# Kernel tuning notes

Measured on AMD Instinct MI355X. Metric: run time of the kernel, lower is better.

Reference implementation:

```python
import jax, jax.numpy as jnp
import numpy as np


def setup_inputs() -> dict:
    key = jax.random.key(0)
    ks = jax.random.split(key, 7)
    C = 256
    Cqk = C // 8  # 32
    B, D, H, W = 4, 16, 16, 16
    s_in = 1.0 / np.sqrt(C)  # conv1x1 fan_in = C
    return {
        "x": jax.random.normal(ks[0], (B, C, D, H, W), dtype=jnp.float32),
        "Wq": jax.random.uniform(ks[1], (Cqk, C), jnp.float32, -s_in, s_in),
        "bq": jax.random.uniform(ks[2], (Cqk,), jnp.float32, -s_in, s_in),
        "Wk": jax.random.uniform(ks[3], (Cqk, C), jnp.float32, -s_in, s_in),
        "bk": jax.random.uniform(ks[4], (Cqk,), jnp.float32, -s_in, s_in),
        "Wv": jax.random.uniform(ks[5], (C, C), jnp.float32, -s_in, s_in),
        "bv": jax.random.uniform(ks[6], (C,), jnp.float32, -s_in, s_in),
    }


def reference(x, Wq, bq, Wk, bk, Wv, bv):
    B, C, D, H, W = x.shape
    N = D * H * W
    xf = x.reshape(B, C, N)  # [B, C, N]
    # 1x1x1 convs == per-voxel GEMMs over the channel dim
    q = jnp.einsum('oc,bcn->bon', Wq, xf) + bq[None, :, None]  # [B, Cqk, N]
    k = jnp.einsum('oc,bcn->bon', Wk, xf) + bk[None, :, None]  # [B, Cqk, N]
    v = jnp.einsum('oc,bcn->bon', Wv, xf) + bv[None, :, None]  # [B, C, N]
    # attention[b, n, m] = softmax_m( q[:, n] . k[:, m] )
    scores = jnp.einsum('bcn,bcm->bnm', q, k)  # [B, N, N]
    attn = jax.nn.softmax(scores, axis=-1)
    # out = value @ attention^T  -> out[b, c, n] = sum_m v[b,c,m] * attn[b,n,m]
    out = jnp.einsum('bcm,bnm->bcn', v, attn)
    return x + out.reshape(B, C, D, H, W)
```

## Files before the change

kernel.cpp:

```cpp
#include <hip/hip_runtime.h>
#include <math.h>

#define B_   4
#define C_   256
#define CQK  32
#define N_   4096
#define TQ   64
#define TM   64
#define HITERS ((N_ / 2) / TM)
#define PSS  72
#define VSH  (C_ * TM)
#define XT2  264
#define VOS  40

typedef __attribute__((ext_vector_type(8))) short short8;
typedef __attribute__((ext_vector_type(4))) short short4v;
typedef __attribute__((ext_vector_type(4))) float f32x4;
typedef __attribute__((ext_vector_type(2))) unsigned int uint2v;

#if __has_builtin(__builtin_amdgcn_exp2f)
#define EXP2F(x) __builtin_amdgcn_exp2f(x)
#else
#define EXP2F(x) exp2f(x)
#endif

typedef const __attribute__((address_space(1))) unsigned int* gas1_t;
typedef __attribute__((address_space(3))) unsigned int* las3_t;
__device__ __forceinline__ void gload_lds16(const unsigned short* g, unsigned short* l) {
    __builtin_amdgcn_global_load_lds((gas1_t)g, (las3_t)l, 16, 0, 0);
}

__device__ __forceinline__ unsigned short f2bf(float f) {
    unsigned u = __builtin_bit_cast(unsigned, f);
    u += 0x7fffu + ((u >> 16) & 1u);
    return (unsigned short)(u >> 16);
}
__device__ __forceinline__ float bf2f(unsigned short s) {
    return __builtin_bit_cast(float, (unsigned)s << 16);
}
__device__ __forceinline__ unsigned pack2bf(float a, float b) {
    unsigned ua = __builtin_bit_cast(unsigned, a) + 0x8000u;
    unsigned ub = __builtin_bit_cast(unsigned, b) + 0x8000u;
#if __has_builtin(__builtin_amdgcn_perm)
    return __builtin_amdgcn_perm(ub, ua, 0x07060302u);
#else
    return (ua >> 16) | (ub & 0xffff0000u);
#endif
}

__global__ __launch_bounds__(256) void cvt_w(
    const float* __restrict__ Wq, const float* __restrict__ bq,
    const float* __restrict__ Wk, const float* __restrict__ bk,
    const float* __restrict__ Wv, const float* __restrict__ bv,
    unsigned short* __restrict__ wbf, float* __restrict__ biasf)
{
    const float LOG2E = 1.4426950408889634f;
    const int r = blockIdx.x;
    const int t = threadIdx.x;
    const float* src = (r < 32) ? (Wq + r * C_)
                     : (r < 64) ? (Wk + (r - 32) * C_)
                                : (Wv + (r - 64) * C_);
    const float scale = (r < 32) ? LOG2E : 1.0f;
    wbf[r * C_ + t] = f2bf(src[t] * scale);
    if (t == 0)
        biasf[r] = (r < 32) ? bq[r] * LOG2E : (r < 64) ? bk[r - 32] : bv[r - 64];
}

__global__ __launch_bounds__(256, 2) void proj_qkv(
    const float* __restrict__ x, const unsigned short* __restrict__ wbf,
    const float* __restrict__ biasf,
    unsigned short* __restrict__ qb, unsigned short* __restrict__ kb,
    unsigned short* __restrict__ vb)
{
    __shared__ __align__(16) unsigned short xT[32 * XT2];
    __shared__ __align__(16) unsigned short vout[256 * VOS];
    __shared__ __align__(16) unsigned short qks[32 * 72];

    const int t    = threadIdx.x;
    const int w    = t >> 6;
    const int lane = t & 63;
    const int quad = lane >> 4;
    const int c16  = lane & 15;
    const int n0   = blockIdx.x * 32;
    const int b    = blockIdx.y;

    {
        const int c0 = (t >> 3) * 8;
        const int nq = t & 7;
        f32x4 xv[8];
#pragma unroll
        for (int i = 0; i < 8; ++i)
            xv[i] = *(const f32x4*)&x[((size_t)(b * C_) + c0 + i) * N_ + n0 + 4 * nq];
#pragma unroll
        for (int j = 0; j < 4; ++j) {
            short8 pk;
#pragma unroll
            for (int i = 0; i < 8; ++i) pk[i] = (short)f2bf(xv[i][j]);
            *(short8*)&xT[(4 * nq + j) * XT2 + c0] = pk;
        }
    }
    __syncthreads();

    f32x4 acc[5][2];
#pragma unroll
    for (int i = 0; i < 5; ++i)
#pragma unroll
        for (int nt = 0; nt < 2; ++nt) acc[i][nt] = (f32x4){0.f, 0.f, 0.f, 0.f};

    const unsigned short* wr = wbf + (size_t)(80 * w + c16) * C_ + quad * 8;

#pragma unroll
    for (int ks = 0; ks < 8; ++ks) {
        short8 af[5], bf[2];
#pragma unroll
        for (int i = 0; i < 5; ++i)
            af[i] = *(const short8*)(wr + (size_t)(16 * i) * C_ + 32 * ks);
#pragma unroll
        for (int nt = 0; nt < 2; ++nt)
            bf[nt] = *(const short8*)&xT[(16 * nt + c16) * XT2 + ks * 32 + quad * 8];
#pragma unroll
        for (int i = 0; i < 5; ++i)
#pragma unroll
            for (int nt = 0; nt < 2; ++nt)
                acc[i][nt] = __builtin_amdgcn_mfma_f32_16x16x32_bf16(af[i], bf[nt], acc[i][nt], 0, 0, 0);
    }

#pragma unroll
    for (int i = 0; i < 5; ++i) {
        const int OT = 5 * w + i;
        const int obase = OT * 16 + 4 * quad;
        const f32x4 bv4 = *(const f32x4*)&biasf[obase];
#pragma unroll
        for (int nt = 0; nt < 2; ++nt) {
            const int n = 16 * nt + c16;
            float vals[4];
#pragma unroll
            for (int r = 0; r < 4; ++r) vals[r] = acc[i][nt][r] + bv4[r];
            if (OT >= 4) {
#pragma unroll
                for (int r = 0; r < 4; ++r)
                    vout[(obase + r - 64) * VOS + n] = f2bf(vals[r]);
            } else {
                const int col = (OT < 2 ? 0 : 32) + (OT & 1) * 16 + 4 * quad;
                short4v pk;
#pragma unroll
                for (int r = 0; r < 4; ++r) pk[r] = (short)f2bf(vals[r]);
                *(short4v*)&qks[n * 72 + col] = pk;
            }
        }
    }
    __syncthreads();

#pragma unroll
    for (int p = 0; p < 4; ++p) {
        const int c   = 64 * p + (t >> 2);
        const int seg = t & 3;
        const short8 vv = *(const short8*)&vout[c * VOS + seg * 8];
        *(short8*)(vb + ((size_t)(b * C_) + c) * N_ + n0 + seg * 8) = vv;
    }
    if (w < 2) {
        unsigned short* dst = w ? kb : qb;
        const int coff = w ? 32 : 0;
#pragma unroll
        for (int h = 0; h < 2; ++h) {
            const int n = 16 * h + (lane >> 2);
            const int c = (lane & 3) * 8;
            const short8 v = *(const short8*)&qks[n * 72 + coff + c];
            *(short8*)(dst + ((size_t)(b * N_) + n0 + n) * 32 + c) = v;
        }
    }
}

__global__ __launch_bounds__(512, 4) void attn_kernel(
    const unsigned short* __restrict__ qg,
    const unsigned short* __restrict__ kg,
    const unsigned short* __restrict__ vg,
    float* __restrict__ outp,
    unsigned short* __restrict__ Op1,
    float* __restrict__ lp)
{
    __shared__ __align__(16) unsigned short vs[2 * VSH];
    __shared__ __align__(16) unsigned short ps[TQ * PSS];
    __shared__ float ls[4 * TQ];

    const int t    = threadIdx.x;
    const int w    = t >> 6;
    const int lane = t & 63;
    const int quad = lane >> 4;
    const int c16  = lane & 15;
    const int flat = blockIdx.x;
    const int half = flat & 1;
    const int b    = (flat >> 1) & 3;
    const int q0   = (flat >> 3) * TQ;
    const int kvb0 = half * (N_ / 2);
    const int f   = w & 3;
    const int qg_ = w >> 2;
    const int cs = w & 3;
    const int pg = w >> 2;

    const unsigned short* kbase = kg + (size_t)(b * N_) * 32;
    const unsigned short* vbase = vg + (size_t)(b * C_) * N_;

    short8 bq[2];
#pragma unroll
    for (int g = 0; g < 2; ++g)
        bq[g] = *(const short8*)(qg + ((size_t)(b * N_) + q0 + 16 * (2 * qg_ + g) + c16) * 32 + quad * 8);

    const int vrow  = lane >> 3;
    const int vslot = lane & 7;

    const size_t koff = (size_t)(16 * f + c16) * 32 + quad * 8;

#pragma unroll
    for (int p = 0; p < 4; ++p) {
        const int c = 32 * w + 8 * p + vrow;
        gload_lds16(vbase + (size_t)c * N_ + kvb0 + 8 * (vslot ^ (c & 7)),
                    &vs[(32 * w + 8 * p) * TM]);
    }
    short8 akpre = *(const short8*)(kbase + (size_t)kvb0 * 32 + koff);
    __syncthreads();

    f32x4 O[4][2];
#pragma unroll
    for (int ct = 0; ct < 4; ++ct)
#pragma unroll
        for (int qt = 0; qt < 2; ++qt) O[ct][qt] = (f32x4){0.f, 0.f, 0.f, 0.f};

    float lacc[2] = {0.f, 0.f};

#pragma unroll 1
    for (int it = 0; it < HITERS; ++it) {
        const int cur = it & 1;
        const int nxt = cur ^ 1;

        const f32x4 z = {0.f, 0.f, 0.f, 0.f};
        f32x4 sf[2];
#pragma unroll
        for (int g = 0; g < 2; ++g)
            sf[g] = __builtin_amdgcn_mfma_f32_16x16x32_bf16(akpre, bq[g], z, 0, 0, 0);

#pragma unroll
        for (int g = 0; g < 2; ++g) {
            float p[4];
#pragma unroll
            for (int r = 0; r < 4; ++r) p[r] = EXP2F(sf[g][r]);
            lacc[g] += (p[0] + p[1]) + (p[2] + p[3]);
            uint2v u;
            u.x = pack2bf(p[0], p[1]);
            u.y = pack2bf(p[2], p[3]);
            *(uint2v*)&ps[(16 * (2 * qg_ + g) + c16) * PSS + f * 16 + 4 * quad] = u;
        }
        __syncthreads();

        if (it + 1 < HITERS) {
            const int kv0n = kvb0 + (it + 1) * TM;
#pragma unroll
            for (int p = 0; p < 4; ++p) {
                const int c = 32 * w + 8 * p + vrow;
                gload_lds16(vbase + (size_t)c * N_ + kv0n + 8 * (vslot ^ (c & 7)),
                            &vs[nxt * VSH + (32 * w + 8 * p) * TM]);
            }
            akpre = *(const short8*)(kbase + (size_t)kv0n * 32 + koff);
        }

        short8 bp[2][2];
#pragma unroll
        for (int qt = 0; qt < 2; ++qt)
#pragma unroll
            for (int s = 0; s < 2; ++s)
                bp[qt][s] = *(const short8*)&ps[(32 * pg + 16 * qt + c16) * PSS + 32 * s + 8 * quad];
#pragma unroll
        for (int s = 0; s < 2; ++s)
#pragma unroll
            for (int ct = 0; ct < 4; ++ct) {
                const int c = 64 * cs + 16 * ct + c16;
                const short8 av = *(const short8*)&vs[cur * VSH + c * TM + 8 * ((4 * s + quad) ^ (c & 7))];
#pragma unroll
                for (int qt = 0; qt < 2; ++qt)
                    O[ct][qt] = __builtin_amdgcn_mfma_f32_16x16x32_bf16(av, bp[qt][s], O[ct][qt], 0, 0, 0);
            }
        __syncthreads();
    }

#pragma unroll
    for (int g = 0; g < 2; ++g) {
        lacc[g] += __shfl_xor(lacc[g], 16);
        lacc[g] += __shfl_xor(lacc[g], 32);
    }
    if (quad == 0) {
#pragma unroll
        for (int g = 0; g < 2; ++g)
            ls[f * TQ + 16 * (2 * qg_ + g) + c16] = lacc[g];
    }
    __syncthreads();

    if (half == 0) {
        float* ob = outp + (size_t)(b * C_) * N_;
#pragma unroll
        for (int ct = 0; ct < 4; ++ct)
#pragma unroll
            for (int qt = 0; qt < 2; ++qt) {
                const int n = q0 + 32 * pg + 16 * qt + c16;
#pragma unroll
                for (int r = 0; r < 4; ++r) {
                    const int c = 64 * cs + 16 * ct + 4 * quad + r;
                    ob[(size_t)c * N_ + n] = O[ct][qt][r];
                }
            }
    } else {
        unsigned short* ob = Op1 + (size_t)(b * C_) * N_;
#pragma unroll
        for (int ct = 0; ct < 4; ++ct)
#pragma unroll
            for (int qt = 0; qt < 2; ++qt) {
                const int n = q0 + 32 * pg + 16 * qt + c16;
#pragma unroll
                for (int r = 0; r < 4; ++r) {
                    const int c = 64 * cs + 16 * ct + 4 * quad + r;
                    ob[(size_t)c * N_ + n] = f2bf(O[ct][qt][r]);
                }
            }
    }
    if (w == 0) {
        const int qq = lane;
        const float lv = ls[qq] + ls[TQ + qq] + ls[2 * TQ + qq] + ls[3 * TQ + qq];
        lp[(size_t)(half * B_ + b) * N_ + q0 + qq] = lv;
    }
}

__global__ __launch_bounds__(256) void combine_kernel(
    const float* __restrict__ x,
    const unsigned short* __restrict__ Op1,
    const float* __restrict__ lp,
    float* __restrict__ out)
{
    __shared__ float linv[1024];

    const int t  = threadIdx.x;
    const int n0 = blockIdx.x * 1024;
    const int c0 = blockIdx.y * 8;
    const int b  = blockIdx.z;

#pragma unroll
    for (int i = 0; i < 4; ++i) {
        const int n = n0 + t + 256 * i;
        const float l = lp[(size_t)b * N_ + n] + lp[(size_t)(B_ + b) * N_ + n];
        linv[t + 256 * i] = 1.0f / l;
    }
    __syncthreads();

#pragma unroll
    for (int cc = 0; cc < 8; ++cc) {
        const int c = c0 + cc;
        const size_t base = ((size_t)(b * C_) + c) * N_ + n0 + 4 * t;
        const f32x4 o0 = *(const f32x4*)&out[base];
        const short4v a1 = *(const short4v*)&Op1[base];
        const f32x4 xv = *(const f32x4*)&x[base];
        f32x4 o;
        o.x = xv.x + (o0.x + bf2f((unsigned short)a1[0])) * linv[4 * t + 0];
        o.y = xv.y + (o0.y + bf2f((unsigned short)a1[1])) * linv[4 * t + 1];
        o.z = xv.z + (o0.z + bf2f((unsigned short)a1[2])) * linv[4 * t + 2];
        o.w = xv.w + (o0.w + bf2f((unsigned short)a1[3])) * linv[4 * t + 3];
        *(f32x4*)&out[base] = o;
    }
}

extern "C" void kernel_launch(void* const* d_in, const int* in_sizes, int n_in,
                              void* d_out, int out_size, void* d_ws, size_t ws_size,
                              hipStream_t stream) {
    const float* x  = (const float*)d_in[0];
    const float* Wq = (const float*)d_in[1];
    const float* bq = (const float*)d_in[2];
    const float* Wk = (const float*)d_in[3];
    const float* bk = (const float*)d_in[4];
    const float* Wv = (const float*)d_in[5];
    const float* bv = (const float*)d_in[6];
    float* out = (float*)d_out;

    unsigned short* ws16 = (unsigned short*)d_ws;
    unsigned short* qb  = ws16;
    unsigned short* kb  = qb + (size_t)B_ * N_ * 32;
    unsigned short* vb  = kb + (size_t)B_ * N_ * 32;
    unsigned short* Op1 = vb + (size_t)B_ * C_ * N_;
    unsigned short* wbf = Op1 + (size_t)B_ * C_ * N_;
    float* biasf = (float*)(wbf + 320 * C_);
    float* lpp   = biasf + 320;

    cvt_w<<<dim3(320), 256, 0, stream>>>(Wq, bq, Wk, bk, Wv, bv, wbf, biasf);
    proj_qkv<<<dim3(N_ / 32, B_), 256, 0, stream>>>(x, wbf, biasf, qb, kb, vb);
    attn_kernel<<<dim3(512), 512, 0, stream>>>(qb, kb, vb, out, Op1, lpp);
    combine_kernel<<<dim3(4, 32, B_), 256, 0, stream>>>(x, Op1, lpp, out);
}
```

Baseline: 145.0 us.

## Split KV range four ways with larger query tiles and single-buffered V

```diff
diff --git a/kernel.cpp b/kernel.cpp
--- a/kernel.cpp
+++ b/kernel.cpp
@@ -5,13 +5,16 @@
 #define C_   256
 #define CQK  32
 #define N_   4096
-#define TQ   64
 #define TM   64
-#define HITERS ((N_ / 2) / TM)
 #define PSS  72
 #define VSH  (C_ * TM)
 #define XT2  264
 #define VOS  40
+
+#define TQ2  64
+#define HIT2W ((N_ / 2) / TM)
+#define TQ4  128
+#define HIT4W ((N_ / 4) / TM)
 
 typedef __attribute__((ext_vector_type(8))) short short8;
 typedef __attribute__((ext_vector_type(4))) short short4v;
@@ -171,7 +174,212 @@
     }
 }
 
-__global__ __launch_bounds__(512, 4) void attn_kernel(
+__global__ __launch_bounds__(512, 4) void attn4_kernel(
+    const unsigned short* __restrict__ qg,
+    const unsigned short* __restrict__ kg,
+    const unsigned short* __restrict__ vg,
+    float* __restrict__ outp,
+    unsigned short* __restrict__ Op1,
+    unsigned short* __restrict__ Op2,
+    unsigned short* __restrict__ Op3,
+    float* __restrict__ lp)
+{
+    __shared__ __align__(16) unsigned short vs[VSH];
+    __shared__ __align__(16) unsigned short ps[TQ4 * PSS];
+    __shared__ float ls[4 * TQ4];
+
+    const int t    = threadIdx.x;
+    const int w    = t >> 6;
+    const int lane = t & 63;
+    const int quad = lane >> 4;
+    const int c16  = lane & 15;
+    const int flat = blockIdx.x;
+    const int quarter = flat & 3;
+    const int b    = (flat >> 2) & 3;
+    const int q0   = (flat >> 4) * TQ4;
+    const int kvb0 = quarter * (N_ / 4);
+    const int f   = w & 3;
+    const int qg_ = w >> 2;
+    const int cs = w & 3;
+    const int pg = w >> 2;
+
+    const unsigned short* kbase = kg + (size_t)(b * N_) * 32;
+    const unsigned short* vbase = vg + (size_t)(b * C_) * N_;
+
+    short8 bq[4];
+#pragma unroll
+    for (int g = 0; g < 4; ++g)
+        bq[g] = *(const short8*)(qg + ((size_t)(b * N_) + q0 + 16 * (4 * qg_ + g) + c16) * 32 + quad * 8);
+
+    const int vrow  = lane >> 3;
+    const int vslot = lane & 7;
+    const size_t koff = (size_t)(16 * f + c16) * 32 + quad * 8;
+
+#pragma unroll
+    for (int p = 0; p < 4; ++p) {
+        const int c = 32 * w + 8 * p + vrow;
+        gload_lds16(vbase + (size_t)c * N_ + kvb0 + 8 * (vslot ^ (c & 7)),
+                    &vs[(32 * w + 8 * p) * TM]);
+    }
+    short8 akpre = *(const short8*)(kbase + (size_t)kvb0 * 32 + koff);
+
+    f32x4 O[4][4];
+#pragma unroll
+    for (int ct = 0; ct < 4; ++ct)
+#pragma unroll
+        for (int qt = 0; qt < 4; ++qt) O[ct][qt] = (f32x4){0.f, 0.f, 0.f, 0.f};
+
+    float lacc[4] = {0.f, 0.f, 0.f, 0.f};
+
+#pragma unroll 1
+    for (int it = 0; it < HIT4W; ++it) {
+        if (it > 0) {
+            const int kv0 = kvb0 + it * TM;
+#pragma unroll
+            for (int p = 0; p < 4; ++p) {
+                const int c = 32 * w + 8 * p + vrow;
+                gload_lds16(vbase + (size_t)c * N_ + kv0 + 8 * (vslot ^ (c & 7)),
+                            &vs[(32 * w + 8 * p) * TM]);
+            }
+        }
+
+        const f32x4 z = {0.f, 0.f, 0.f, 0.f};
+        f32x4 sf[4];
+#pragma unroll
+        for (int g = 0; g < 4; ++g)
+            sf[g] = __builtin_amdgcn_mfma_f32_16x16x32_bf16(akpre, bq[g], z, 0, 0, 0);
+
+        if (it + 1 < HIT4W)
+            akpre = *(const short8*)(kbase + (size_t)(kvb0 + (it + 1) * TM) * 32 + koff);
+
+#pragma unroll
+        for (int g = 0; g < 4; ++g) {
+            float p[4];
+#pragma unroll
+            for (int r = 0; r < 4; ++r) p[r] = EXP2F(sf[g][r]);
+            lacc[g] += (p[0] + p[1]) + (p[2] + p[3]);
+            uint2v u;
+            u.x = pack2bf(p[0], p[1]);
+            u.y = pack2bf(p[2], p[3]);
+            *(uint2v*)&ps[(16 * (4 * qg_ + g) + c16) * PSS + f * 16 + 4 * quad] = u;
+        }
+        __syncthreads();
+
+        short8 bp[4][2];
+#pragma unroll
+        for (int qt = 0; qt < 4; ++qt)
+#pragma unroll
+            for (int s = 0; s < 2; ++s)
+                bp[qt][s] = *(const short8*)&ps[(64 * pg + 16 * qt + c16) * PSS + 32 * s + 8 * quad];
+#pragma unroll
+        for (int s = 0; s < 2; ++s)
+#pragma unroll
+            for (int ct = 0; ct < 4; ++ct) {
+                const int c = 64 * cs + 16 * ct + c16;
+                const short8 av = *(const short8*)&vs[c * TM + 8 * ((4 * s + quad) ^ (c & 7))];
+#pragma unroll
+                for (int qt = 0; qt < 4; ++qt)
+                    O[ct][qt] = __builtin_amdgcn_mfma_f32_16x16x32_bf16(av, bp[qt][s], O[ct][qt], 0, 0, 0);
+            }
+        __syncthreads();
+    }
+
+#pragma unroll
+    for (int g = 0; g < 4; ++g) {
+        lacc[g] += __shfl_xor(lacc[g], 16);
+        lacc[g] += __shfl_xor(lacc[g], 32);
+    }
+    if (quad == 0) {
+#pragma unroll
+        for (int g = 0; g < 4; ++g)
+            ls[f * TQ4 + 16 * (4 * qg_ + g) + c16] = lacc[g];
+    }
+    __syncthreads();
+
+    if (quarter == 0) {
+        float* ob = outp + (size_t)(b * C_) * N_;
+#pragma unroll
+        for (int ct = 0; ct < 4; ++ct)
+#pragma unroll
+            for (int qt = 0; qt < 4; ++qt) {
+                const int n = q0 + 64 * pg + 16 * qt + c16;
+#pragma unroll
+                for (int r = 0; r < 4; ++r) {
+                    const int c = 64 * cs + 16 * ct + 4 * quad + r;
+                    ob[(size_t)c * N_ + n] = O[ct][qt][r];
+                }
+            }
+    } else {
+        unsigned short* op = (quarter == 1) ? Op1 : (quarter == 2) ? Op2 : Op3;
+        unsigned short* ob = op + (size_t)(b * C_) * N_;
+#pragma unroll
+        for (int ct = 0; ct < 4; ++ct)
+#pragma unroll
+            for (int qt = 0; qt < 4; ++qt) {
+                const int n = q0 + 64 * pg + 16 * qt + c16;
+#pragma unroll
+                for (int r = 0; r < 4; ++r) {
+                    const int c = 64 * cs + 16 * ct + 4 * quad + r;
+                    ob[(size_t)c * N_ + n] = f2bf(O[ct][qt][r]);
+                }
+            }
+    }
+    if (w == 0) {
+#pragma unroll
+        for (int h = 0; h < 2; ++h) {
+            const int qq = lane + 64 * h;
+            const float lv = ls[qq] + ls[TQ4 + qq] + ls[2 * TQ4 + qq] + ls[3 * TQ4 + qq];
+            lp[(size_t)(quarter * B_ + b) * N_ + q0 + qq] = lv;
+        }
+    }
+}
+
+__global__ __launch_bounds__(256) void combine4_kernel(
+    const float* __restrict__ x,
+    const unsigned short* __restrict__ Op1,
+    const unsigned short* __restrict__ Op2,
+    const unsigned short* __restrict__ Op3,
+    const float* __restrict__ lp,
+    float* __restrict__ out)
+{
+    __shared__ float linv[1024];
+
+    const int t  = threadIdx.x;
+    const int n0 = blockIdx.x * 1024;
+    const int c0 = blockIdx.y * 8;
+    const int b  = blockIdx.z;
+
+#pragma unroll
+    for (int i = 0; i < 4; ++i) {
+        const int n = n0 + t + 256 * i;
+        float l = 0.f;
+#pragma unroll
+        for (int q = 0; q < 4; ++q) l += lp[(size_t)(q * B_ + b) * N_ + n];
+        linv[t + 256 * i] = 1.0f / l;
+    }
+    __syncthreads();
+
+#pragma unroll
+    for (int cc = 0; cc < 8; ++cc) {
+        const int c = c0 + cc;
+        const size_t base = ((size_t)(b * C_) + c) * N_ + n0 + 4 * t;
+        const f32x4 o0 = *(const f32x4*)&out[base];
+        const short4v a1 = *(const short4v*)&Op1[base];
+        const short4v a2 = *(const short4v*)&Op2[base];
+        const short4v a3 = *(const short4v*)&Op3[base];
+        const f32x4 xv = *(const f32x4*)&x[base];
+        f32x4 o;
+#pragma unroll
+        for (int r = 0; r < 4; ++r) {
+            const float s = o0[r] + bf2f((unsigned short)a1[r]) + bf2f((unsigned short)a2[r])
+                                  + bf2f((unsigned short)a3[r]);
+            o[r] = xv[r] + s * linv[4 * t + r];
+        }
+        *(f32x4*)&out[base] = o;
+    }
+}
+
+__global__ __launch_bounds__(512, 4) void attn2_kernel(
     const unsigned short* __restrict__ qg,
     const unsigned short* __restrict__ kg,
     const unsigned short* __restrict__ vg,
@@ -180,8 +388,8 @@
     float* __restrict__ lp)
 {
     __shared__ __align__(16) unsigned short vs[2 * VSH];
-    __shared__ __align__(16) unsigned short ps[TQ * PSS];
-    __shared__ float ls[4 * TQ];
+    __shared__ __align__(16) unsigned short ps[TQ2 * PSS];
+    __shared__ float ls[4 * TQ2];
 
     const int t    = threadIdx.x;
     const int w    = t >> 6;
@@ -191,7 +399,7 @@
     const int flat = blockIdx.x;
     const int half = flat & 1;
     const int b    = (flat >> 1) & 3;
-    const int q0   = (flat >> 3) * TQ;
+    const int q0   = (flat >> 3) * TQ2;
     const int kvb0 = half * (N_ / 2);
     const int f   = w & 3;
     const int qg_ = w >> 2;
@@ -208,7 +416,6 @@
 
     const int vrow  = lane >> 3;
     const int vslot = lane & 7;
-
     const size_t koff = (size_t)(16 * f + c16) * 32 + quad * 8;
 
 #pragma unroll
@@ -229,7 +436,7 @@
     float lacc[2] = {0.f, 0.f};
 
 #pragma unroll 1
-    for (int it = 0; it < HITERS; ++it) {
+    for (int it = 0; it < HIT2W; ++it) {
         const int cur = it & 1;
         const int nxt = cur ^ 1;
 
@@ -252,7 +459,7 @@
         }
         __syncthreads();
 
-        if (it + 1 < HITERS) {
+        if (it + 1 < HIT2W) {
             const int kv0n = kvb0 + (it + 1) * TM;
 #pragma unroll
             for (int p = 0; p < 4; ++p) {
@@ -260,7 +467,7 @@
                 gload_lds16(vbase + (size_t)c * N_ + kv0n + 8 * (vslot ^ (c & 7)),
                             &vs[nxt * VSH + (32 * w + 8 * p) * TM]);
             }
-            akpre = *(const short8*)(kbase + (size_t)kv0n * 32 + koff);
+            akpre = *(const short8*)(kbase + (size_t)(kv0n) * 32 + koff);
         }
 
         short8 bp[2][2];
@@ -290,7 +497,7 @@
     if (quad == 0) {
 #pragma unroll
         for (int g = 0; g < 2; ++g)
-            ls[f * TQ + 16 * (2 * qg_ + g) + c16] = lacc[g];
+            ls[f * TQ2 + 16 * (2 * qg_ + g) + c16] = lacc[g];
     }
     __syncthreads();
 
@@ -323,12 +530,12 @@
     }
     if (w == 0) {
         const int qq = lane;
-        const float lv = ls[qq] + ls[TQ + qq] + ls[2 * TQ + qq] + ls[3 * TQ + qq];
+        const float lv = ls[qq] + ls[TQ2 + qq] + ls[2 * TQ2 + qq] + ls[3 * TQ2 + qq];
         lp[(size_t)(half * B_ + b) * N_ + q0 + qq] = lv;
     }
 }
 
-__global__ __launch_bounds__(256) void combine_kernel(
+__global__ __launch_bounds__(256) void combine2_kernel(
     const float* __restrict__ x,
     const unsigned short* __restrict__ Op1,
     const float* __restrict__ lp,
@@ -377,17 +584,33 @@
     const float* bv = (const float*)d_in[6];
     float* out = (float*)d_out;
 
+    const size_t SZ_QKB = (size_t)B_ * N_ * 32;
+    const size_t SZ_CN  = (size_t)B_ * C_ * N_;
+
     unsigned short* ws16 = (unsigned short*)d_ws;
     unsigned short* qb  = ws16;
-    unsigned short* kb  = qb + (size_t)B_ * N_ * 32;
-    unsigned short* vb  = kb + (size_t)B_ * N_ * 32;
-    unsigned short* Op1 = vb + (size_t)B_ * C_ * N_;
-    unsigned short* wbf = Op1 + (size_t)B_ * C_ * N_;
-    float* biasf = (float*)(wbf + 320 * C_);
-    float* lpp   = biasf + 320;
-
-    cvt_w<<<dim3(320), 256, 0, stream>>>(Wq, bq, Wk, bk, Wv, bv, wbf, biasf);
-    proj_qkv<<<dim3(N_ / 32, B_), 256, 0, stream>>>(x, wbf, biasf, qb, kb, vb);
-    attn_kernel<<<dim3(512), 512, 0, stream>>>(qb, kb, vb, out, Op1, lpp);
-    combine_kernel<<<dim3(4, 32, B_), 256, 0, stream>>>(x, Op1, lpp, out);
-}
+    unsigned short* kb  = qb + SZ_QKB;
+    unsigned short* vb  = kb + SZ_QKB;
+    unsigned short* Op1 = vb + SZ_CN;
+    unsigned short* Op2 = Op1 + SZ_CN;
+    unsigned short* Op3 = Op2 + SZ_CN;
+    const size_t need4 = (2 * SZ_QKB + 4 * SZ_CN + 320 * C_) * 2 + 320 * 4 + (size_t)4 * B_ * N_ * 4 + 1024;
+
+    if (ws_size >= need4) {
+        unsigned short* wbf = Op3 + SZ_CN;
+        float* biasf = (float*)(wbf + 320 * C_);
+        float* lpp   = biasf + 320;
+        cvt_w<<<dim3(320), 256, 0, stream>>>(Wq, bq, Wk, bk, Wv, bv, wbf, biasf);
+        proj_qkv<<<dim3(N_ / 32, B_), 256, 0, stream>>>(x, wbf, biasf, qb, kb, vb);
+        attn4_kernel<<<dim3(512), 512, 0, stream>>>(qb, kb, vb, out, Op1, Op2, Op3, lpp);
+        combine4_kernel<<<dim3(4, 32, B_), 256, 0, stream>>>(x, Op1, Op2, Op3, lpp, out);
+    } else {
+        unsigned short* wbf = Op1 + SZ_CN;
+        float* biasf = (float*)(wbf + 320 * C_);
+        float* lpp   = biasf + 320;
+        cvt_w<<<dim3(320), 256, 0, stream>>>(Wq, bq, Wk, bk, Wv, bv, wbf, biasf);
+        proj_qkv<<<dim3(N_ / 32, B_), 256, 0, stream>>>(x, wbf, biasf, qb, kb, vb);
+        attn2_kernel<<<dim3(512), 512, 0, stream>>>(qb, kb, vb, out, Op1, lpp);
+        combine2_kernel<<<dim3(4, 32, B_), 256, 0, stream>>>(x, Op1, lpp, out);
+    }
+}
```

New measurement: 157.9 us. 1.09x slower.
